# Kernel tuning notes

Hardware: AMD Instinct MI355X
Metric: run time of the kernel (lower is better)

## Reference

```python
import jax, jax.numpy as jnp
import numpy as np

N = 100000   # nodes
E = 1600000  # edges
IN = 128
HID = 64
HEADS = 2
OUT = 16
G = 100      # graphs in batch
NEG_SLOPE = 0.2


def setup_inputs() -> dict:
    key = jax.random.key(0)
    ks = jax.random.split(key, 14)
    s = 0.05
    return {
        "x": jax.random.normal(ks[0], (N, IN), jnp.float32),
        "edge_index": jax.random.randint(ks[1], (2, E), 0, N, dtype=jnp.int32),
        "batch": jnp.sort(jax.random.randint(ks[2], (N,), 0, G, dtype=jnp.int32)),
        "W1": jax.random.normal(ks[3], (IN, HEADS * HID), jnp.float32) * s,
        "att_src1": jax.random.normal(ks[4], (HEADS, HID), jnp.float32) * s,
        "att_dst1": jax.random.normal(ks[5], (HEADS, HID), jnp.float32) * s,
        "b1": jax.random.normal(ks[6], (HEADS * HID,), jnp.float32) * s,
        "W2": jax.random.normal(ks[7], (HEADS * HID, HID), jnp.float32) * s,
        "att_src2": jax.random.normal(ks[8], (1, HID), jnp.float32) * s,
        "att_dst2": jax.random.normal(ks[9], (1, HID), jnp.float32) * s,
        "b2": jax.random.normal(ks[10], (HID,), jnp.float32) * s,
        "Wl": jax.random.normal(ks[11], (HID, OUT), jnp.float32) * s,
        "bl": jax.random.normal(ks[12], (OUT,), jnp.float32) * s,
    }


def gat_conv(x, src, dst, W, a_src, a_dst, b, heads, out_c):
    """PyG GATConv: transform, per-edge attention, segment softmax over dst, scatter-add."""
    n = x.shape[0]
    h = (x @ W).reshape(n, heads, out_c)              # [N, H, C]
    alpha_src = (h * a_src).sum(-1)                   # [N, H]
    alpha_dst = (h * a_dst).sum(-1)                   # [N, H]
    e = jax.nn.leaky_relu(alpha_src[src] + alpha_dst[dst], NEG_SLOPE)  # [Etot, H]
    m = jax.ops.segment_max(e, dst, num_segments=n)   # stable softmax per dst
    ex = jnp.exp(e - m[dst])
    den = jax.ops.segment_sum(ex, dst, num_segments=n)
    alpha = ex / den[dst]                             # [Etot, H]
    msg = h[src] * alpha[..., None]                   # [Etot, H, C]
    out = jax.ops.segment_sum(msg, dst, num_segments=n)
    return out.reshape(n, heads * out_c) + b


def reference(x, edge_index, batch, W1, att_src1, att_dst1, b1,
              W2, att_src2, att_dst2, b2, Wl, bl):
    n = x.shape[0]
    loop = jnp.arange(n, dtype=edge_index.dtype)      # PyG add_self_loops default
    src = jnp.concatenate([edge_index[0], loop])
    dst = jnp.concatenate([edge_index[1], loop])
    h = gat_conv(x, src, dst, W1, att_src1, att_dst1, b1, HEADS, HID)
    h = jax.nn.relu(h)
    h = gat_conv(h, src, dst, W2, att_src2, att_dst2, b2, 1, HID)
    sums = jax.ops.segment_sum(h, batch, num_segments=G)
    cnt = jax.ops.segment_sum(jnp.ones((n,), h.dtype), batch, num_segments=G)
    pooled = sums / jnp.maximum(cnt, 1.0)[:, None]    # global_mean_pool
    return pooled @ Wl + bl
```

## Files before the change

kernel.cpp:

```cpp
#include <hip/hip_runtime.h>
#include <math.h>

#define GRAPHS 100
#define HIDC 64
#define OUTC 16
#define SLOPE 0.2f
#define BSHIFT 8
#define MAXNB 512
#define BKT_CAP 10240

typedef unsigned short ushort_t;
typedef short bf16x8 __attribute__((ext_vector_type(8)));
typedef float f32x4 __attribute__((ext_vector_type(4)));
typedef ushort_t u16x8 __attribute__((ext_vector_type(8)));
typedef ushort_t u16x4 __attribute__((ext_vector_type(4)));

__device__ __forceinline__ float lrelu(float v) { return v > 0.f ? v : SLOPE * v; }
__device__ __forceinline__ void atomAddG(float* p, float v) { unsafeAtomicAdd(p, v); }
__device__ __forceinline__ float bf2f(ushort_t u) {
    unsigned int x = ((unsigned int)u) << 16;
    return __builtin_bit_cast(float, x);
}
__device__ __forceinline__ ushort_t f2bf(float f) {
    unsigned int u = __builtin_bit_cast(unsigned int, f);
    u += 0x7FFFu + ((u >> 16) & 1u);
    return (ushort_t)(u >> 16);
}
__device__ __forceinline__ unsigned int pack2(float lo, float hi) {
    return (unsigned int)f2bf(lo) | ((unsigned int)f2bf(hi) << 16);
}

template <bool A_IS_BF16>
__global__ __launch_bounds__(256) void mfma_gemm(const void* __restrict__ Av,
                                                 const float* __restrict__ W,
                                                 ushort_t* __restrict__ Cbf,
                                                 int M, int K, int N) {
    __shared__ ushort_t As[64 * 40];
    __shared__ ushort_t Bs[64 * 40];
    const int tid = threadIdx.x;
    const int row0 = blockIdx.x * 64;
    const int col0 = blockIdx.y * 64;
    const int lane = tid & 63;
    const int wv = tid >> 6;
    const int wr = (wv >> 1) * 32, wc = (wv & 1) * 32;
    const int l15 = lane & 15, l4 = lane >> 4;

    const int srow = tid >> 2;
    const int skoff = (tid & 3) * 8;
    const int bc = tid & 63, bk = (tid >> 6) * 8;

    f32x4 acc[2][2] = {};

    for (int k0 = 0; k0 < K; k0 += 32) {
        {
            int gr = row0 + srow;
            uint4 v = {0u, 0u, 0u, 0u};
            if (gr < M) {
                if (A_IS_BF16) {
                    const ushort_t* Ab = (const ushort_t*)Av;
                    v = *(const uint4*)(Ab + (size_t)gr * K + k0 + skoff);
                } else {
                    const float* Af = (const float*)Av;
                    const float4 a0 = *(const float4*)(Af + (size_t)gr * K + k0 + skoff);
                    const float4 a1 = *(const float4*)(Af + (size_t)gr * K + k0 + skoff + 4);
                    v.x = pack2(a0.x, a0.y);
                    v.y = pack2(a0.z, a0.w);
                    v.z = pack2(a1.x, a1.y);
                    v.w = pack2(a1.z, a1.w);
                }
            }
            *(uint4*)&As[srow * 40 + skoff] = v;
        }
        {
#pragma unroll
            for (int j = 0; j < 8; ++j) {
                float w = W[(size_t)(k0 + bk + j) * N + col0 + bc];
                Bs[bc * 40 + bk + j] = f2bf(w);
            }
        }
        __syncthreads();
        bf16x8 af[2], bfr[2];
#pragma unroll
        for (int mi = 0; mi < 2; ++mi)
            af[mi] = *(const bf16x8*)&As[(wr + mi * 16 + l15) * 40 + l4 * 8];
#pragma unroll
        for (int ni = 0; ni < 2; ++ni)
            bfr[ni] = *(const bf16x8*)&Bs[(wc + ni * 16 + l15) * 40 + l4 * 8];
#pragma unroll
        for (int mi = 0; mi < 2; ++mi)
#pragma unroll
            for (int ni = 0; ni < 2; ++ni)
                acc[mi][ni] = __builtin_amdgcn_mfma_f32_16x16x32_bf16(af[mi], bfr[ni],
                                                                     acc[mi][ni], 0, 0, 0);
        __syncthreads();
    }
#pragma unroll
    for (int mi = 0; mi < 2; ++mi)
#pragma unroll
        for (int ni = 0; ni < 2; ++ni)
#pragma unroll
            for (int r = 0; r < 4; ++r) {
                int row = row0 + wr + mi * 16 + l4 * 4 + r;
                int colg = col0 + wc + ni * 16 + l15;
                if (row < M) Cbf[(size_t)row * N + colg] = f2bf(acc[mi][ni][r]);
            }
}

__global__ void alpha1_kernel(const ushort_t* __restrict__ h, const float* __restrict__ att_src,
                              const float* __restrict__ att_dst, float* __restrict__ asrc,
                              float* __restrict__ adst, int n) {
    int lane = threadIdx.x & 63;
    int wid = (blockIdx.x * blockDim.x + threadIdx.x) >> 6;
    int nw = (gridDim.x * blockDim.x) >> 6;
    float as0 = att_src[2 * lane], as1 = att_src[2 * lane + 1];
    float ad0 = att_dst[2 * lane], ad1 = att_dst[2 * lane + 1];
    for (int i = wid; i < n; i += nw) {
        ushort2 v = *(const ushort2*)(h + (size_t)i * 128 + 2 * lane);
        float v0 = bf2f(v.x), v1 = bf2f(v.y);
        float s = v0 * as0 + v1 * as1;
        float d = v0 * ad0 + v1 * ad1;
#pragma unroll
        for (int off = 16; off; off >>= 1) {
            s += __shfl_xor(s, off);
            d += __shfl_xor(d, off);
        }
        if ((lane & 31) == 0) {
            int hd = lane >> 5;
            asrc[2 * i + hd] = s;
            adst[2 * i + hd] = d;
        }
    }
}

__global__ void alpha2_kernel(const ushort_t* __restrict__ h, const float* __restrict__ att_src,
                              const float* __restrict__ att_dst, float* __restrict__ asrc,
                              float* __restrict__ adst, int n) {
    int lane = threadIdx.x & 63;
    int wid = (blockIdx.x * blockDim.x + threadIdx.x) >> 6;
    int nw = (gridDim.x * blockDim.x) >> 6;
    float asc = att_src[lane], adc = att_dst[lane];
    for (int i = wid; i < n; i += nw) {
        float v = bf2f(h[(size_t)i * 64 + lane]);
        float s = v * asc, d = v * adc;
#pragma unroll
        for (int off = 32; off; off >>= 1) {
            s += __shfl_xor(s, off);
            d += __shfl_xor(d, off);
        }
        if (lane == 0) {
            asrc[i] = s;
            adst[i] = d;
        }
    }
}

__global__ __launch_bounds__(256) void bucket_hist(const int* __restrict__ ei, int E,
                                                   int* __restrict__ bcnt, int NB) {
    __shared__ int h[MAXNB];
    for (int t = threadIdx.x; t < NB; t += 256) h[t] = 0;
    __syncthreads();
    int chunk = (E + gridDim.x - 1) / gridDim.x;
    int e0 = blockIdx.x * chunk;
    int e1 = e0 + chunk < E ? e0 + chunk : E;
    for (int e = e0 + threadIdx.x; e < e1; e += 256)
        atomicAdd(&h[ei[E + e] >> BSHIFT], 1);
    __syncthreads();
    for (int t = threadIdx.x; t < NB; t += 256)
        if (h[t]) atomicAdd(&bcnt[t], h[t]);
}

__global__ __launch_bounds__(512) void bucket_scan(const int* __restrict__ bcnt,
                                                   int* __restrict__ bbase,
                                                   int* __restrict__ bcursor,
                                                   int* __restrict__ rowptr,
                                                   int NB, int n, int E) {
    __shared__ int sh[512];
    int t = threadIdx.x;
    int v = (t < NB) ? bcnt[t] : 0;
    sh[t] = v;
    __syncthreads();
#pragma unroll
    for (int off = 1; off < 512; off <<= 1) {
        int val = (t >= off) ? sh[t - off] : 0;
        __syncthreads();
        sh[t] += val;
        __syncthreads();
    }
    if (t < NB) {
        int base = sh[t] - v;
        bbase[t] = base;
        bcursor[t] = base;
    }
    if (t == 0) {
        bbase[NB] = E;
        rowptr[n] = E;
    }
}

__global__ __launch_bounds__(256) void bucket_scatter(const int* __restrict__ ei, int E,
                                                      int* __restrict__ bcursor,
                                                      unsigned int* __restrict__ ebuf, int NB) {
    __shared__ int h[MAXNB];
    __shared__ int lbase[MAXNB];
    for (int t = threadIdx.x; t < NB; t += 256) h[t] = 0;
    __syncthreads();
    int chunk = (E + gridDim.x - 1) / gridDim.x;
    int e0 = blockIdx.x * chunk;
    int e1 = e0 + chunk < E ? e0 + chunk : E;
    for (int e = e0 + threadIdx.x; e < e1; e += 256)
        atomicAdd(&h[ei[E + e] >> BSHIFT], 1);
    __syncthreads();
    for (int t = threadIdx.x; t < NB; t += 256) {
        int c = h[t];
        lbase[t] = c ? atomicAdd(&bcursor[t], c) : 0;
        h[t] = 0;
    }
    __syncthreads();
    for (int e = e0 + threadIdx.x; e < e1; e += 256) {
        int d = ei[E + e];
        int s = ei[e];
        int b = d >> BSHIFT;
        int off = atomicAdd(&h[b], 1);
        ebuf[lbase[b] + off] = (unsigned)s | ((unsigned)(d & ((1 << BSHIFT) - 1)) << 24);
    }
}

__global__ __launch_bounds__(256) void bucket_build(const unsigned int* __restrict__ ebuf,
                                                    const int* __restrict__ bbase,
                                                    int* __restrict__ rowptr,
                                                    int* __restrict__ col, int n) {
    __shared__ int hist[256];
    __shared__ int curs[256];
    __shared__ int sh[256];
    __shared__ int lsrc[BKT_CAP];
    int b = blockIdx.x;
    int e0 = bbase[b], e1 = bbase[b + 1];
    int cnt = e1 - e0;
    int t = threadIdx.x;
    hist[t] = 0;
    __syncthreads();
    for (int k = t; k < cnt; k += 256) atomicAdd(&hist[ebuf[e0 + k] >> 24], 1);
    __syncthreads();
    int v = hist[t];
    sh[t] = v;
    __syncthreads();
#pragma unroll
    for (int off = 1; off < 256; off <<= 1) {
        int val = (t >= off) ? sh[t - off] : 0;
        __syncthreads();
        sh[t] += val;
        __syncthreads();
    }
    int ex = sh[t] - v;
    curs[t] = ex;
    int node = (b << BSHIFT) + t;
    if (node < n) rowptr[node] = e0 + ex;
    __syncthreads();
    for (int k = t; k < cnt; k += 256) {
        unsigned pk = ebuf[e0 + k];
        int ld = pk >> 24;
        int off = atomicAdd(&curs[ld], 1);
        if (off < BKT_CAP) lsrc[off] = (int)(pk & 0xFFFFFFu);
    }
    __syncthreads();
    int lim = cnt < BKT_CAP ? cnt : BKT_CAP;
    for (int k = t; k < lim; k += 256) col[e0 + k] = lsrc[k];
}

__global__ __launch_bounds__(256) void gat_agg1(const int* __restrict__ rowptr,
                                                const int* __restrict__ col,
                                                const ushort_t* __restrict__ h,
                                                const float* __restrict__ asrc,
                                                const float* __restrict__ adst,
                                                const float* __restrict__ b1,
                                                ushort_t* __restrict__ outb, int n) {
    int i = (blockIdx.x * blockDim.x + threadIdx.x) >> 6;
    if (i >= n) return;
    int lane = threadIdx.x & 63;
    int grp = lane >> 4, c = lane & 15;
    int head = c >> 3;
    float ad = adst[2 * i + head];
    const u16x8* h8 = (const u16x8*)h;
    float acc[8] = {};
    float den = 0.f;
    if (grp == 0) {
        float w = __expf(lrelu(asrc[2 * i + head] + ad));
        u16x8 hv = h8[(size_t)i * 16 + c];
#pragma unroll
        for (int j = 0; j < 8; ++j) acc[j] = bf2f(hv[j]) * w;
        den = w;
    }
    int e0 = rowptr[i], end = rowptr[i + 1];
    for (int e = e0; e < end; e += 8) {
        int iA = e + grp, iB = e + 4 + grp;
        bool vA = iA < end, vB = iB < end;
        int sA = col[vA ? iA : e0];
        int sB = col[vB ? iB : e0];
        float asA = asrc[2 * sA + head];
        float asB = asrc[2 * sB + head];
        u16x8 hA = h8[(size_t)sA * 16 + c];
        u16x8 hB = h8[(size_t)sB * 16 + c];
        float wA = vA ? __expf(lrelu(asA + ad)) : 0.f;
        float wB = vB ? __expf(lrelu(asB + ad)) : 0.f;
#pragma unroll
        for (int j = 0; j < 8; ++j) acc[j] = fmaf(bf2f(hA[j]), wA, acc[j]);
#pragma unroll
        for (int j = 0; j < 8; ++j) acc[j] = fmaf(bf2f(hB[j]), wB, acc[j]);
        den += wA + wB;
    }
#pragma unroll
    for (int j = 0; j < 8; ++j) {
        acc[j] += __shfl_xor(acc[j], 16);
        acc[j] += __shfl_xor(acc[j], 32);
    }
    den += __shfl_xor(den, 16);
    den += __shfl_xor(den, 32);
    if (grp == 0) {
        float inv = 1.f / den;
        u16x8 ov;
#pragma unroll
        for (int j = 0; j < 8; ++j) {
            float r = fmaf(acc[j], inv, b1[8 * c + j]);
            r = r > 0.f ? r : 0.f;
            ov[j] = f2bf(r);
        }
        *((u16x8*)outb + (size_t)i * 16 + c) = ov;
    }
}

__global__ __launch_bounds__(256) void gat_agg2(const int* __restrict__ rowptr,
                                                const int* __restrict__ col,
                                                const ushort_t* __restrict__ h,
                                                const float* __restrict__ asrc,
                                                const float* __restrict__ adst,
                                                float* __restrict__ outb, int n) {
    int i = (blockIdx.x * blockDim.x + threadIdx.x) >> 6;
    if (i >= n) return;
    int lane = threadIdx.x & 63;
    int grp = lane >> 4, c = lane & 15;
    float ad = adst[i];
    const u16x4* h4 = (const u16x4*)h;
    float acc[4] = {};
    float den = 0.f;
    if (grp == 0) {
        float w = __expf(lrelu(asrc[i] + ad));
        u16x4 hv = h4[(size_t)i * 16 + c];
#pragma unroll
        for (int j = 0; j < 4; ++j) acc[j] = bf2f(hv[j]) * w;
        den = w;
    }
    int e0 = rowptr[i], end = rowptr[i + 1];
    for (int e = e0; e < end; e += 8) {
        int iA = e + grp, iB = e + 4 + grp;
        bool vA = iA < end, vB = iB < end;
        int sA = col[vA ? iA : e0];
        int sB = col[vB ? iB : e0];
        float asA = asrc[sA];
        float asB = asrc[sB];
        u16x4 hA = h4[(size_t)sA * 16 + c];
        u16x4 hB = h4[(size_t)sB * 16 + c];
        float wA = vA ? __expf(lrelu(asA + ad)) : 0.f;
        float wB = vB ? __expf(lrelu(asB + ad)) : 0.f;
#pragma unroll
        for (int j = 0; j < 4; ++j) acc[j] = fmaf(bf2f(hA[j]), wA, acc[j]);
#pragma unroll
        for (int j = 0; j < 4; ++j) acc[j] = fmaf(bf2f(hB[j]), wB, acc[j]);
        den += wA + wB;
    }
#pragma unroll
    for (int j = 0; j < 4; ++j) {
        acc[j] += __shfl_xor(acc[j], 16);
        acc[j] += __shfl_xor(acc[j], 32);
    }
    den += __shfl_xor(den, 16);
    den += __shfl_xor(den, 32);
    if (grp == 0) {
        float inv = 1.f / den;
        float4 o = {acc[0] * inv, acc[1] * inv, acc[2] * inv, acc[3] * inv};
        *((float4*)outb + (size_t)i * 16 + c) = o;
    }
}

#define NPB 256
__global__ __launch_bounds__(256) void pool_kernel(const float* __restrict__ h,
                                                   const int* __restrict__ batch,
                                                   float* __restrict__ sums,
                                                   float* __restrict__ cnt, int n) {
    __shared__ float ls[GRAPHS * HIDC];
    __shared__ float lc[GRAPHS];
    int base = blockIdx.x * NPB;
    for (int t = threadIdx.x; t < GRAPHS * HIDC; t += blockDim.x) ls[t] = 0.f;
    for (int t = threadIdx.x; t < GRAPHS; t += blockDim.x) lc[t] = 0.f;
    __syncthreads();
    int wave = threadIdx.x >> 6, lane = threadIdx.x & 63;
    int end = base + NPB < n ? base + NPB : n;
    for (int i = base + wave; i < end; i += 4) {
        int g = batch[i];
        unsafeAtomicAdd(&ls[g * HIDC + lane], h[(size_t)i * HIDC + lane]);
        if (lane == 0) unsafeAtomicAdd(&lc[g], 1.f);
    }
    __syncthreads();
    int gmin = batch[base];
    int gmax = batch[end - 1];
    int ng = gmax - gmin + 1;
    for (int t = threadIdx.x; t < ng * HIDC; t += blockDim.x) {
        int g = gmin + t / HIDC, c = t % HIDC;
        atomAddG(&sums[g * HIDC + c], ls[g * HIDC + c]);
    }
    for (int g = gmin + (int)threadIdx.x; g <= gmax; g += blockDim.x)
        atomAddG(&cnt[g], lc[g]);
}

__global__ void final_kernel(const float* __restrict__ sums, const float* __restrict__ cnt,
                             const float* __restrict__ b2, const float* __restrict__ Wl,
                             const float* __restrict__ bl, float* __restrict__ out) {
    int t = blockIdx.x * blockDim.x + threadIdx.x;
    if (t < GRAPHS * OUTC) {
        int g = t / OUTC, o = t % OUTC;
        float c = cnt[g];
        c = c > 1.f ? c : 1.f;
        float inv = 1.f / c;
        float acc = bl[o];
        for (int k = 0; k < HIDC; ++k)
            acc += (sums[g * HIDC + k] * inv + b2[k]) * Wl[k * OUTC + o];
        out[t] = acc;
    }
}

extern "C" void kernel_launch(void* const* d_in, const int* in_sizes, int n_in, void* d_out,
                              int out_size, void* d_ws, size_t ws_size, hipStream_t stream) {
    const float* x = (const float*)d_in[0];
    const int* ei = (const int*)d_in[1];
    const int* batch = (const int*)d_in[2];
    const float* W1 = (const float*)d_in[3];
    const float* att_src1 = (const float*)d_in[4];
    const float* att_dst1 = (const float*)d_in[5];
    const float* b1 = (const float*)d_in[6];
    const float* W2 = (const float*)d_in[7];
    const float* att_src2 = (const float*)d_in[8];
    const float* att_dst2 = (const float*)d_in[9];
    const float* b2 = (const float*)d_in[10];
    const float* Wl = (const float*)d_in[11];
    const float* bl = (const float*)d_in[12];
    float* out = (float*)d_out;

    const int n = in_sizes[2];
    const int E = in_sizes[1] / 2;

    char* p = (char*)d_ws;
    auto alloc = [&](size_t bytes) {
        char* r = p;
        p += (bytes + 255) & ~(size_t)255;
        return r;
    };
    ushort_t* h1 = (ushort_t*)alloc((size_t)n * 128 * 2);
    ushort_t* hrelu = (ushort_t*)alloc((size_t)n * 128 * 2);
    ushort_t* h2 = (ushort_t*)alloc((size_t)n * 64 * 2);
    float* conv2 = (float*)alloc((size_t)n * 64 * 4);
    float* asrc1 = (float*)alloc((size_t)n * 2 * 4);
    float* adst1 = (float*)alloc((size_t)n * 2 * 4);
    float* asrc2 = (float*)alloc((size_t)n * 4);
    float* adst2 = (float*)alloc((size_t)n * 4);
    float* sums = (float*)alloc(GRAPHS * HIDC * 4);
    float* cnt = (float*)alloc(GRAPHS * 4);
    int* bcnt = (int*)alloc(MAXNB * 4);
    int* bbase = (int*)alloc((MAXNB + 1) * 4);
    int* bcursor = (int*)alloc(MAXNB * 4);
    int* rowptr = (int*)alloc(((size_t)n + 1) * 4);
    unsigned int* ebuf = (unsigned int*)alloc((size_t)E * 4);
    int* col = (int*)alloc((size_t)E * 4);

    const int NB = (n + 255) >> BSHIFT;
    const int gblk = (n + 63) / 64;

    hipMemsetAsync(bcnt, 0, NB * sizeof(int), stream);
    bucket_hist<<<512, 256, 0, stream>>>(ei, E, bcnt, NB);
    bucket_scan<<<1, 512, 0, stream>>>(bcnt, bbase, bcursor, rowptr, NB, n, E);
    bucket_scatter<<<512, 256, 0, stream>>>(ei, E, bcursor, ebuf, NB);
    bucket_build<<<NB, 256, 0, stream>>>(ebuf, bbase, rowptr, col, n);

    mfma_gemm<false><<<dim3(gblk, 2), 256, 0, stream>>>(x, W1, h1, n, 128, 128);
    alpha1_kernel<<<2048, 256, 0, stream>>>(h1, att_src1, att_dst1, asrc1, adst1, n);
    gat_agg1<<<(n + 3) / 4, 256, 0, stream>>>(rowptr, col, h1, asrc1, adst1, b1, hrelu, n);

    mfma_gemm<true><<<dim3(gblk, 1), 256, 0, stream>>>(hrelu, W2, h2, n, 128, 64);
    alpha2_kernel<<<2048, 256, 0, stream>>>(h2, att_src2, att_dst2, asrc2, adst2, n);
    gat_agg2<<<(n + 3) / 4, 256, 0, stream>>>(rowptr, col, h2, asrc2, adst2, conv2, n);

    hipMemsetAsync(sums, 0, (GRAPHS * HIDC + GRAPHS) * sizeof(float), stream);
    pool_kernel<<<(n + NPB - 1) / NPB, 256, 0, stream>>>(conv2, batch, sums, cnt, n);
    final_kernel<<<(GRAPHS * OUTC + 255) / 256, 256, 0, stream>>>(sums, cnt, b2, Wl, bl, out);
}
```

Before: 396.4 us.

## Fuse attention logits into GEMM epilogue, deepen gather unroll, store conv2 in bf16

Computes the per-node attention dot products (asrc/adst) inside the MFMA GEMM epilogue from the fp32 accumulators. A shuffle reduction plus a small shared-memory combine replaces the separate alpha kernels that re-read h from memory. The aggregation loops now issue four neighbor gathers per iteration instead of two, which puts more loads in flight. conv2 is stored as bf16, halving its write and the pool read, at some precision cost, and the logits now come from unrounded accumulators instead of bf16 h.

After: 363.2 us. 8.4% less time.

```diff
diff --git a/kernel.cpp b/kernel.cpp
--- a/kernel.cpp
+++ b/kernel.cpp
@@ -30,13 +30,18 @@
     return (unsigned int)f2bf(lo) | ((unsigned int)f2bf(hi) << 16);
 }
 
-template <bool A_IS_BF16>
-__global__ __launch_bounds__(256) void mfma_gemm(const void* __restrict__ Av,
-                                                 const float* __restrict__ W,
-                                                 ushort_t* __restrict__ Cbf,
-                                                 int M, int K, int N) {
+template <bool A_IS_BF16, int ASTRIDE>
+__global__ __launch_bounds__(256) void mfma_gemm_alpha(const void* __restrict__ Av,
+                                                       const float* __restrict__ W,
+                                                       ushort_t* __restrict__ Cbf,
+                                                       const float* __restrict__ att_src,
+                                                       const float* __restrict__ att_dst,
+                                                       float* __restrict__ asrc,
+                                                       float* __restrict__ adst,
+                                                       int M, int K, int N) {
     __shared__ ushort_t As[64 * 40];
     __shared__ ushort_t Bs[64 * 40];
+    __shared__ float ps[2][64], pd[2][64];
     const int tid = threadIdx.x;
     const int row0 = blockIdx.x * 64;
     const int col0 = blockIdx.y * 64;
@@ -104,52 +109,36 @@
                 int colg = col0 + wc + ni * 16 + l15;
                 if (row < M) Cbf[(size_t)row * N + colg] = f2bf(acc[mi][ni][r]);
             }
-}
-
-__global__ void alpha1_kernel(const ushort_t* __restrict__ h, const float* __restrict__ att_src,
-                              const float* __restrict__ att_dst, float* __restrict__ asrc,
-                              float* __restrict__ adst, int n) {
-    int lane = threadIdx.x & 63;
-    int wid = (blockIdx.x * blockDim.x + threadIdx.x) >> 6;
-    int nw = (gridDim.x * blockDim.x) >> 6;
-    float as0 = att_src[2 * lane], as1 = att_src[2 * lane + 1];
-    float ad0 = att_dst[2 * lane], ad1 = att_dst[2 * lane + 1];
-    for (int i = wid; i < n; i += nw) {
-        ushort2 v = *(const ushort2*)(h + (size_t)i * 128 + 2 * lane);
-        float v0 = bf2f(v.x), v1 = bf2f(v.y);
-        float s = v0 * as0 + v1 * as1;
-        float d = v0 * ad0 + v1 * ad1;
-#pragma unroll
-        for (int off = 16; off; off >>= 1) {
-            s += __shfl_xor(s, off);
-            d += __shfl_xor(d, off);
-        }
-        if ((lane & 31) == 0) {
-            int hd = lane >> 5;
-            asrc[2 * i + hd] = s;
-            adst[2 * i + hd] = d;
-        }
-    }
-}
-
-__global__ void alpha2_kernel(const ushort_t* __restrict__ h, const float* __restrict__ att_src,
-                              const float* __restrict__ att_dst, float* __restrict__ asrc,
-                              float* __restrict__ adst, int n) {
-    int lane = threadIdx.x & 63;
-    int wid = (blockIdx.x * blockDim.x + threadIdx.x) >> 6;
-    int nw = (gridDim.x * blockDim.x) >> 6;
-    float asc = att_src[lane], adc = att_dst[lane];
-    for (int i = wid; i < n; i += nw) {
-        float v = bf2f(h[(size_t)i * 64 + lane]);
-        float s = v * asc, d = v * adc;
-#pragma unroll
-        for (int off = 32; off; off >>= 1) {
-            s += __shfl_xor(s, off);
-            d += __shfl_xor(d, off);
-        }
-        if (lane == 0) {
-            asrc[i] = s;
-            adst[i] = d;
+    float as_c[2], ad_c[2];
+#pragma unroll
+    for (int ni = 0; ni < 2; ++ni) {
+        int cidx = col0 + wc + ni * 16 + l15;
+        as_c[ni] = att_src[cidx];
+        ad_c[ni] = att_dst[cidx];
+    }
+#pragma unroll
+    for (int mi = 0; mi < 2; ++mi)
+#pragma unroll
+        for (int r = 0; r < 4; ++r) {
+            float s = acc[mi][0][r] * as_c[0] + acc[mi][1][r] * as_c[1];
+            float d = acc[mi][0][r] * ad_c[0] + acc[mi][1][r] * ad_c[1];
+#pragma unroll
+            for (int off = 1; off < 16; off <<= 1) {
+                s += __shfl_xor(s, off);
+                d += __shfl_xor(d, off);
+            }
+            if (l15 == 0) {
+                int rl = wr + mi * 16 + l4 * 4 + r;
+                ps[wc >> 5][rl] = s;
+                pd[wc >> 5][rl] = d;
+            }
+        }
+    __syncthreads();
+    if (tid < 64) {
+        int row = row0 + tid;
+        if (row < M) {
+            asrc[ASTRIDE * row + blockIdx.y] = ps[0][tid] + ps[1][tid];
+            adst[ASTRIDE * row + blockIdx.y] = pd[0][tid] + pd[1][tid];
         }
     }
 }
@@ -291,22 +280,24 @@
         den = w;
     }
     int e0 = rowptr[i], end = rowptr[i + 1];
-    for (int e = e0; e < end; e += 8) {
-        int iA = e + grp, iB = e + 4 + grp;
-        bool vA = iA < end, vB = iB < end;
-        int sA = col[vA ? iA : e0];
-        int sB = col[vB ? iB : e0];
-        float asA = asrc[2 * sA + head];
-        float asB = asrc[2 * sB + head];
-        u16x8 hA = h8[(size_t)sA * 16 + c];
-        u16x8 hB = h8[(size_t)sB * 16 + c];
-        float wA = vA ? __expf(lrelu(asA + ad)) : 0.f;
-        float wB = vB ? __expf(lrelu(asB + ad)) : 0.f;
-#pragma unroll
-        for (int j = 0; j < 8; ++j) acc[j] = fmaf(bf2f(hA[j]), wA, acc[j]);
-#pragma unroll
-        for (int j = 0; j < 8; ++j) acc[j] = fmaf(bf2f(hB[j]), wB, acc[j]);
-        den += wA + wB;
+    for (int e = e0; e < end; e += 16) {
+        float wv[4];
+        u16x8 hv[4];
+#pragma unroll
+        for (int q = 0; q < 4; ++q) {
+            int idx = e + 4 * q + grp;
+            bool vld = idx < end;
+            int s = col[vld ? idx : e0];
+            float as = asrc[2 * s + head];
+            hv[q] = h8[(size_t)s * 16 + c];
+            wv[q] = vld ? __expf(lrelu(as + ad)) : 0.f;
+        }
+#pragma unroll
+        for (int q = 0; q < 4; ++q) {
+#pragma unroll
+            for (int j = 0; j < 8; ++j) acc[j] = fmaf(bf2f(hv[q][j]), wv[q], acc[j]);
+            den += wv[q];
+        }
     }
 #pragma unroll
     for (int j = 0; j < 8; ++j) {
@@ -333,7 +324,7 @@
                                                 const ushort_t* __restrict__ h,
                                                 const float* __restrict__ asrc,
                                                 const float* __restrict__ adst,
-                                                float* __restrict__ outb, int n) {
+                                                ushort_t* __restrict__ outb, int n) {
     int i = (blockIdx.x * blockDim.x + threadIdx.x) >> 6;
     if (i >= n) return;
     int lane = threadIdx.x & 63;
@@ -350,22 +341,24 @@
         den = w;
     }
     int e0 = rowptr[i], end = rowptr[i + 1];
-    for (int e = e0; e < end; e += 8) {
-        int iA = e + grp, iB = e + 4 + grp;
-        bool vA = iA < end, vB = iB < end;
-        int sA = col[vA ? iA : e0];
-        int sB = col[vB ? iB : e0];
-        float asA = asrc[sA];
-        float asB = asrc[sB];
-        u16x4 hA = h4[(size_t)sA * 16 + c];
-        u16x4 hB = h4[(size_t)sB * 16 + c];
-        float wA = vA ? __expf(lrelu(asA + ad)) : 0.f;
-        float wB = vB ? __expf(lrelu(asB + ad)) : 0.f;
-#pragma unroll
-        for (int j = 0; j < 4; ++j) acc[j] = fmaf(bf2f(hA[j]), wA, acc[j]);
-#pragma unroll
-        for (int j = 0; j < 4; ++j) acc[j] = fmaf(bf2f(hB[j]), wB, acc[j]);
-        den += wA + wB;
+    for (int e = e0; e < end; e += 16) {
+        float wv[4];
+        u16x4 hv[4];
+#pragma unroll
+        for (int q = 0; q < 4; ++q) {
+            int idx = e + 4 * q + grp;
+            bool vld = idx < end;
+            int s = col[vld ? idx : e0];
+            float as = asrc[s];
+            hv[q] = h4[(size_t)s * 16 + c];
+            wv[q] = vld ? __expf(lrelu(as + ad)) : 0.f;
+        }
+#pragma unroll
+        for (int q = 0; q < 4; ++q) {
+#pragma unroll
+            for (int j = 0; j < 4; ++j) acc[j] = fmaf(bf2f(hv[q][j]), wv[q], acc[j]);
+            den += wv[q];
+        }
     }
 #pragma unroll
     for (int j = 0; j < 4; ++j) {
@@ -376,13 +369,14 @@
     den += __shfl_xor(den, 32);
     if (grp == 0) {
         float inv = 1.f / den;
-        float4 o = {acc[0] * inv, acc[1] * inv, acc[2] * inv, acc[3] * inv};
-        *((float4*)outb + (size_t)i * 16 + c) = o;
+        u16x4 ov = {f2bf(acc[0] * inv), f2bf(acc[1] * inv), f2bf(acc[2] * inv),
+                    f2bf(acc[3] * inv)};
+        *((u16x4*)outb + (size_t)i * 16 + c) = ov;
     }
 }
 
 #define NPB 256
-__global__ __launch_bounds__(256) void pool_kernel(const float* __restrict__ h,
+__global__ __launch_bounds__(256) void pool_kernel(const ushort_t* __restrict__ h,
                                                    const int* __restrict__ batch,
                                                    float* __restrict__ sums,
                                                    float* __restrict__ cnt, int n) {
@@ -396,7 +390,7 @@
     int end = base + NPB < n ? base + NPB : n;
     for (int i = base + wave; i < end; i += 4) {
         int g = batch[i];
-        unsafeAtomicAdd(&ls[g * HIDC + lane], h[(size_t)i * HIDC + lane]);
+        unsafeAtomicAdd(&ls[g * HIDC + lane], bf2f(h[(size_t)i * HIDC + lane]));
         if (lane == 0) unsafeAtomicAdd(&lc[g], 1.f);
     }
     __syncthreads();
@@ -456,7 +450,7 @@
     ushort_t* h1 = (ushort_t*)alloc((size_t)n * 128 * 2);
     ushort_t* hrelu = (ushort_t*)alloc((size_t)n * 128 * 2);
     ushort_t* h2 = (ushort_t*)alloc((size_t)n * 64 * 2);
-    float* conv2 = (float*)alloc((size_t)n * 64 * 4);
+    ushort_t* conv2 = (ushort_t*)alloc((size_t)n * 64 * 2);
     float* asrc1 = (float*)alloc((size_t)n * 2 * 4);
     float* adst1 = (float*)alloc((size_t)n * 2 * 4);
     float* asrc2 = (float*)alloc((size_t)n * 4);
@@ -479,12 +473,12 @@
     bucket_scatter<<<512, 256, 0, stream>>>(ei, E, bcursor, ebuf, NB);
     bucket_build<<<NB, 256, 0, stream>>>(ebuf, bbase, rowptr, col, n);
 
-    mfma_gemm<false><<<dim3(gblk, 2), 256, 0, stream>>>(x, W1, h1, n, 128, 128);
-    alpha1_kernel<<<2048, 256, 0, stream>>>(h1, att_src1, att_dst1, asrc1, adst1, n);
+    mfma_gemm_alpha<false, 2><<<dim3(gblk, 2), 256, 0, stream>>>(
+        x, W1, h1, att_src1, att_dst1, asrc1, adst1, n, 128, 128);
     gat_agg1<<<(n + 3) / 4, 256, 0, stream>>>(rowptr, col, h1, asrc1, adst1, b1, hrelu, n);
 
-    mfma_gemm<true><<<dim3(gblk, 1), 256, 0, stream>>>(hrelu, W2, h2, n, 128, 64);
-    alpha2_kernel<<<2048, 256, 0, stream>>>(h2, att_src2, att_dst2, asrc2, adst2, n);
+    mfma_gemm_alpha<true, 1><<<dim3(gblk, 1), 256, 0, stream>>>(
+        hrelu, W2, h2, att_src2, att_dst2, asrc2, adst2, n, 128, 64);
     gat_agg2<<<(n + 3) / 4, 256, 0, stream>>>(rowptr, col, h2, asrc2, adst2, conv2, n);
 
     hipMemsetAsync(sums, 0, (GRAPHS * HIDC + GRAPHS) * sizeof(float), stream);
```
